# Optimization experiments

Measured on AMD Instinct MI355X. Metric: run time of the kernel, lower is better.

Reference implementation:

```python
import jax, jax.numpy as jnp
import numpy as np

N_HEADS = 8
WINDOW = 4

def setup_inputs() -> dict:
    key = jax.random.key(0)
    ks = jax.random.split(key, 12)
    B, C, L = 8, 512, 1024
    Dh = C // N_HEADS
    s = 1.0 / np.sqrt(C)
    inp = {
        'x': jax.random.normal(ks[0], (B, C, L), dtype=jnp.float32),
        'Wq': jax.random.normal(ks[1], (C, C), dtype=jnp.float32) * s,
        'bq': jnp.zeros((C,), dtype=jnp.float32),
        'Wk': jax.random.normal(ks[2], (C, C), dtype=jnp.float32) * s,
        'bk': jnp.zeros((C,), dtype=jnp.float32),
        'Wv': jax.random.normal(ks[3], (C, C), dtype=jnp.float32) * s,
        'bv': jnp.zeros((C,), dtype=jnp.float32),
        'Wo': jax.random.normal(ks[4], (C, C), dtype=jnp.float32) * s,
        'bo': jnp.zeros((C,), dtype=jnp.float32),
        'emb_rel_k': jax.random.normal(ks[5], (2 * WINDOW + 1, Dh), dtype=jnp.float32) * 0.02,
        'emb_rel_v': jax.random.normal(ks[6], (2 * WINDOW + 1, Dh), dtype=jnp.float32) * 0.02,
    }
    return inp


def reference(x, Wq, bq, Wk, bk, Wv, bv, Wo, bo, emb_rel_k, emb_rel_v):
    B, C, L = x.shape
    H = N_HEADS
    Dh = C // H
    scale = Dh ** -0.5

    def proj(W, b):
        # pointwise conv1d == channel-mixing matmul; (B,C,L) -> (B,H,L,Dh)
        y = jnp.einsum('oc,bcl->bol', W, x) + b[:, None]
        return y.reshape(B, H, Dh, L).transpose(0, 1, 3, 2)

    q = proj(Wq, bq) * scale
    k = proj(Wk, bk)
    v = proj(Wv, bv)

    scores = jnp.einsum('bhld,bhjd->bhlj', q, k)  # (B,H,L,L)

    t = jnp.arange(L)
    diff = t[None, :] - t[:, None]                      # (L,L)
    window_mask = (jnp.abs(diff) <= WINDOW)
    indices = jnp.clip(diff, -WINDOW, WINDOW) + WINDOW  # (L,L) in [0, 2w]

    rel_k = emb_rel_k[indices]                          # (L,L,Dh)
    rel_scores = jnp.einsum('bhld,ljd->bhlj', q, rel_k)
    scores = scores + rel_scores * window_mask[None, None, :, :]

    attn = jax.nn.softmax(scores, axis=-1)

    out = jnp.einsum('bhlj,bhjd->bhld', attn, v)
    rel_v = emb_rel_v[indices] * window_mask[:, :, None]  # (L,L,Dh)
    out = out + jnp.einsum('bhlj,ljd->bhld', attn, rel_v)

    out = out.transpose(0, 1, 3, 2).reshape(B, C, L)
    out = jnp.einsum('oc,bcl->bol', Wo, out) + bo[:, None]
    return out
```

## Files before the change

kernel.cpp:

```cpp
#include <hip/hip_runtime.h>
#include <math.h>

#define B_  8
#define H_  8
#define C_  512
#define L_  1024
#define DH  64
#define WIN 4

typedef __attribute__((ext_vector_type(8))) short short8;
typedef __attribute__((ext_vector_type(4))) float floatx4;

__device__ __forceinline__ unsigned short f2bf(float f) {
    unsigned int u = __float_as_uint(f);
    u = u + 0x7FFFu + ((u >> 16) & 1u);
    return (unsigned short)(u >> 16);
}
__device__ __forceinline__ float bf2f(unsigned short h) {
    return __uint_as_float(((unsigned int)h) << 16);
}
__device__ __forceinline__ unsigned short f2h(float f) {
    _Float16 h = (_Float16)f;
    return *reinterpret_cast<unsigned short*>(&h);
}

__device__ __forceinline__ void gload_lds16(const void* g, void* l) {
    __builtin_amdgcn_global_load_lds(
        (const __attribute__((address_space(1))) void*)g,
        (__attribute__((address_space(3))) void*)l, 16, 0, 0);
}

__global__ __launch_bounds__(256) void prep_kernel(
    const float* __restrict__ Wq, const float* __restrict__ Wk,
    const float* __restrict__ Wv, const float* __restrict__ Wo,
    const float* __restrict__ bq, const float* __restrict__ bk,
    const float* __restrict__ bv,
    unsigned short* __restrict__ Wqkv_hi,
    unsigned short* __restrict__ Wo_h,
    float* __restrict__ bqkv)
{
    const int i = blockIdx.x * 256 + threadIdx.x;
    float4 v; ushort4 h;

    v = ((const float4*)Wq)[i];
    h.x = f2bf(v.x); h.y = f2bf(v.y); h.z = f2bf(v.z); h.w = f2bf(v.w);
    ((ushort4*)Wqkv_hi)[i] = h;

    v = ((const float4*)Wk)[i];
    h.x = f2bf(v.x); h.y = f2bf(v.y); h.z = f2bf(v.z); h.w = f2bf(v.w);
    ((ushort4*)Wqkv_hi)[65536 + i] = h;

    v = ((const float4*)Wv)[i];
    h.x = f2bf(v.x); h.y = f2bf(v.y); h.z = f2bf(v.z); h.w = f2bf(v.w);
    ((ushort4*)Wqkv_hi)[131072 + i] = h;

    v = ((const float4*)Wo)[i];
    h.x = f2h(v.x); h.y = f2h(v.y); h.z = f2h(v.z); h.w = f2h(v.w);
    ((ushort4*)Wo_h)[i] = h;

    if (i < 512)       bqkv[i] = bq[i];
    else if (i < 1024) bqkv[i] = bk[i - 512];
    else if (i < 1536) bqkv[i] = bv[i - 1024];
}

__global__ __launch_bounds__(256) void transpose_kernel(
    const float* __restrict__ x, unsigned short* __restrict__ xT)
{
    __shared__ float tile[32][33];
    const int b  = blockIdx.z;
    const int cb = blockIdx.y * 32;
    const int lb = blockIdx.x * 32;
    const int t  = threadIdx.x;
    {
        const int l = t & 31, c0 = t >> 5;
#pragma unroll
        for (int p = 0; p < 4; ++p) {
            const int c = c0 + 8 * p;
            tile[c][l] = x[((size_t)b * C_ + cb + c) * L_ + lb + l];
        }
    }
    __syncthreads();
    {
        const int c = t & 31, l0 = t >> 5;
#pragma unroll
        for (int p = 0; p < 4; ++p) {
            const int l = l0 + 8 * p;
            xT[((size_t)b * L_ + lb + l) * C_ + cb + c] = f2bf(tile[c][l]);
        }
    }
}

__global__ __launch_bounds__(256) void qkv_gemm_kernel(
    const unsigned short* __restrict__ Wh, const float* __restrict__ bqkv,
    const unsigned short* __restrict__ xT,
    unsigned short* __restrict__ Qb, unsigned short* __restrict__ Kb,
    unsigned short* __restrict__ Vc)
{
    __shared__ __align__(16) unsigned short SM[18432];

    const int b   = blockIdx.z;
    const int oB  = blockIdx.y * 128;
    const int mat = oB >> 9;
    const int ob  = oB & 511;
    const int lb  = blockIdx.x * 128;
    const int t  = threadIdx.x;
    const int w = t >> 6, lane = t & 63, quad = lane >> 4, lc = lane & 15;
    const int wm = w >> 1, wn = w & 1;

    const unsigned short* Wm = Wh + (size_t)mat * C_ * C_;

    floatx4 acc[4][4];
#pragma unroll
    for (int i = 0; i < 4; ++i)
#pragma unroll
        for (int j = 0; j < 4; ++j) acc[i][j] = (floatx4)0.f;

    const int srow = w * 32 + (lane >> 2);
    const int sc8  = (lane & 3) * 8;

#define QKV_STAGE(BUF, S) {                                                  \
    const int c0_ = (S) * 32;                                                \
    _Pragma("unroll")                                                        \
    for (int p_ = 0; p_ < 2; ++p_) {                                         \
        gload_lds16(&Wm[(size_t)(ob + srow + 16 * p_) * C_ + c0_ + sc8],     \
                    &SM[(0 * 2 + (BUF)) * 4096 + (w * 32 + p_ * 16) * 32]);  \
        gload_lds16(&xT[((size_t)b * L_ + lb + srow + 16 * p_) * C_ + c0_ + sc8], \
                    &SM[(1 * 2 + (BUF)) * 4096 + (w * 32 + p_ * 16) * 32]);  \
    }                                                                        \
}

    QKV_STAGE(0, 0)
    __syncthreads();

    for (int s = 0; s < 16; ++s) {
        const int cur = s & 1;
        if (s < 15) QKV_STAGE(1 - cur, s + 1)

        const unsigned short (*At)[32] =
            reinterpret_cast<const unsigned short (*)[32]>(&SM[(0 * 2 + cur) * 4096]);
        const unsigned short (*Bt)[32] =
            reinterpret_cast<const unsigned short (*)[32]>(&SM[(1 * 2 + cur) * 4096]);

        short8 a[4], bb[4];
#pragma unroll
        for (int mt = 0; mt < 4; ++mt)
            a[mt] = *reinterpret_cast<const short8*>(&At[wm * 64 + mt * 16 + lc][quad * 8]);
#pragma unroll
        for (int nt = 0; nt < 4; ++nt)
            bb[nt] = *reinterpret_cast<const short8*>(&Bt[wn * 64 + nt * 16 + lc][quad * 8]);
#pragma unroll
        for (int mt = 0; mt < 4; ++mt)
#pragma unroll
            for (int nt = 0; nt < 4; ++nt)
                acc[mt][nt] = __builtin_amdgcn_mfma_f32_16x16x32_bf16(
                    a[mt], bb[nt], acc[mt][nt], 0, 0, 0);

        __syncthreads();
    }

    if (mat == 2) {
#pragma unroll
        for (int mt = 0; mt < 4; ++mt) {
#pragma unroll
            for (int r = 0; r < 4; ++r) {
                const int o  = ob + wm * 64 + mt * 16 + quad * 4 + r;
                const float bi = bqkv[1024 + o];
#pragma unroll
                for (int nt = 0; nt < 4; ++nt) {
                    const int l = lb + wn * 64 + nt * 16 + lc;
                    Vc[((size_t)b * C_ + o) * L_ + l] = f2bf(acc[mt][nt][r] + bi);
                }
            }
        }
    } else {
        const float scale = (mat == 0) ? 0.125f : 1.0f;
        unsigned short* dst = (mat == 0) ? Qb : Kb;
        unsigned short (*sT)[144] =
            reinterpret_cast<unsigned short (*)[144]>(&SM[0]);

#pragma unroll
        for (int mt = 0; mt < 4; ++mt) {
#pragma unroll
            for (int r = 0; r < 4; ++r) {
                const int o  = ob + wm * 64 + mt * 16 + quad * 4 + r;
                const float bi = bqkv[mat * 512 + o];
                const int d  = mt * 16 + quad * 4 + r;
#pragma unroll
                for (int nt = 0; nt < 4; ++nt) {
                    const int l = wn * 64 + nt * 16 + lc;
                    sT[l][wm * 72 + d] = f2bf((acc[mt][nt][r] + bi) * scale);
                }
            }
        }
        __syncthreads();
        {
            const int l = t >> 1, hf = t & 1;
#pragma unroll
            for (int h01 = 0; h01 < 2; ++h01) {
                const int hgl = (ob >> 6) + h01;
                const size_t o = (((size_t)b * H_ + hgl) * L_ + lb + l) * DH + hf * 32;
                const int cbase = h01 * 72 + hf * 32;
                uint4 v0 = *reinterpret_cast<const uint4*>(&sT[l][cbase]);
                uint4 v1 = *reinterpret_cast<const uint4*>(&sT[l][cbase + 8]);
                uint4 v2 = *reinterpret_cast<const uint4*>(&sT[l][cbase + 16]);
                uint4 v3 = *reinterpret_cast<const uint4*>(&sT[l][cbase + 24]);
                *reinterpret_cast<uint4*>(&dst[o])      = v0;
                *reinterpret_cast<uint4*>(&dst[o + 8])  = v1;
                *reinterpret_cast<uint4*>(&dst[o + 16]) = v2;
                *reinterpret_cast<uint4*>(&dst[o + 24]) = v3;
            }
        }
    }
}

__global__ __launch_bounds__(512, 4) void attn_kernel12(
    const unsigned short* __restrict__ Qb,
    const unsigned short* __restrict__ Kb,
    const unsigned short* __restrict__ Vc,
    const float* __restrict__ erel_k, const float* __restrict__ erel_v,
    unsigned short* __restrict__ AOh)
{
    __shared__ __align__(16) unsigned short kst[2][64][68];
    __shared__ __align__(16) unsigned short vst[2][64][68];
    __shared__ __align__(16) unsigned short Pl[8][16][68];
    __shared__ float rs[128][9];
    __shared__ float rv[128][9];

    const int t  = threadIdx.x;
    const int bh = blockIdx.x;
    const int rt = blockIdx.y;
    const int b = bh >> 3, h = bh & 7;
    const int w = t >> 6, lane = t & 63, quad = lane >> 4, lc = lane & 15;
    const int row0 = rt * 128;
    const int rowW = row0 + w * 16;

    const size_t qkBase = (size_t)bh * L_ * DH;
    const size_t vBase  = ((size_t)b * C_ + h * DH) * L_;

    for (int i = lane; i < 16 * 9; i += 64) rv[w * 16 + i / 9][i % 9] = 0.f;

    short8 af[2];
#pragma unroll
    for (int kk = 0; kk < 2; ++kk)
        af[kk] = *reinterpret_cast<const short8*>(
            &Qb[qkBase + (size_t)(rowW + lc) * DH + kk * 32 + quad * 8]);

    {
        floatx4 rsa = (floatx4)0.f;
        const int drow = (lc < 9) ? lc : 8;
#pragma unroll
        for (int kk = 0; kk < 2; ++kk) {
            short8 bfr;
#pragma unroll
            for (int i = 0; i < 8; ++i)
                bfr[i] = (short)f2bf(erel_k[drow * 64 + kk * 32 + quad * 8 + i]);
            rsa = __builtin_amdgcn_mfma_f32_16x16x32_bf16(af[kk], bfr, rsa, 0, 0, 0);
        }
        if (lc < 9) {
#pragma unroll
            for (int r = 0; r < 4; ++r)
                rs[w * 16 + quad * 4 + r][lc] = rsa[r];
        }
    }

    const int jr = t >> 3, jc = (t & 7) * 8;
    *reinterpret_cast<uint4*>(&kst[0][jr][jc]) =
        *reinterpret_cast<const uint4*>(&Kb[qkBase + (size_t)jr * DH + jc]);
    *reinterpret_cast<uint4*>(&vst[0][jr][jc]) =
        *reinterpret_cast<const uint4*>(&Vc[vBase + (size_t)jr * L_ + jc]);
    __syncthreads();

    short8 ones;
#pragma unroll
    for (int j = 0; j < 8; ++j) ones[j] = (short)0x3F80;

    floatx4 acc_o[4], acc_l = (floatx4)0.f;
#pragma unroll
    for (int nt = 0; nt < 4; ++nt) acc_o[nt] = (floatx4)0.f;

    for (int jt = 0; jt < L_ / 64; ++jt) {
        const int j0  = jt * 64;
        const int cur = jt & 1;

        uint4 pk, pv;
        if (jt < L_ / 64 - 1) {
            const int j0n = j0 + 64;
            pk = *reinterpret_cast<const uint4*>(
                &Kb[qkBase + (size_t)(j0n + jr) * DH + jc]);
            pv = *reinterpret_cast<const uint4*>(
                &Vc[vBase + (size_t)jr * L_ + j0n + jc]);
        }

        floatx4 sacc[4];
#pragma unroll
        for (int nt = 0; nt < 4; ++nt) sacc[nt] = (floatx4)0.f;
#pragma unroll
        for (int nt = 0; nt < 4; ++nt)
#pragma unroll
            for (int kk = 0; kk < 2; ++kk) {
                const short8 kf = *reinterpret_cast<const short8*>(
                    &kst[cur][nt * 16 + lc][kk * 32 + quad * 8]);
                sacc[nt] = __builtin_amdgcn_mfma_f32_16x16x32_bf16(kf, af[kk], sacc[nt], 0, 0, 0);
            }

        const bool nearD = (j0 <= rowW + 15 + WIN) && (j0 + 63 >= rowW - WIN);
        if (nearD) {
#pragma unroll
            for (int nt = 0; nt < 4; ++nt) {
#pragma unroll
                for (int r = 0; r < 4; ++r) {
                    const int diff = (j0 + nt * 16 + quad * 4 + r) - (rowW + lc);
                    if (diff >= -WIN && diff <= WIN)
                        sacc[nt][r] += rs[w * 16 + lc][diff + WIN];
                }
            }
        }

#pragma unroll
        for (int nt = 0; nt < 4; ++nt) {
            const float e0 = __expf(sacc[nt][0]);
            const float e1 = __expf(sacc[nt][1]);
            const float e2 = __expf(sacc[nt][2]);
            const float e3 = __expf(sacc[nt][3]);
            unsigned int u01, u23;
            asm("v_cvt_pk_bf16_f32 %0, %1, %2" : "=v"(u01) : "v"(e0), "v"(e1));
            asm("v_cvt_pk_bf16_f32 %0, %1, %2" : "=v"(u23) : "v"(e2), "v"(e3));
            uint2 pr; pr.x = u01; pr.y = u23;
            *reinterpret_cast<uint2*>(&Pl[w][lc][nt * 16 + quad * 4]) = pr;
        }

        if (nearD) {
            for (int idx = lane; idx < 16 * 9; idx += 64) {
                const int r16 = idx / 9, dr = idx % 9;
                const int jg = rowW + r16 + dr - WIN;
                if (jg >= j0 && jg < j0 + 64 && jg >= 0 && jg < L_)
                    rv[w * 16 + r16][dr] += bf2f(Pl[w][r16][jg - j0]);
            }
        }

        short8 pf[2];
#pragma unroll
        for (int kk = 0; kk < 2; ++kk)
            pf[kk] = *reinterpret_cast<const short8*>(&Pl[w][lc][kk * 32 + quad * 8]);

#pragma unroll
        for (int kk = 0; kk < 2; ++kk)
            acc_l = __builtin_amdgcn_mfma_f32_16x16x32_bf16(pf[kk], ones, acc_l, 0, 0, 0);

#pragma unroll
        for (int nt = 0; nt < 4; ++nt)
#pragma unroll
            for (int kk = 0; kk < 2; ++kk) {
                const short8 vf = *reinterpret_cast<const short8*>(
                    &vst[cur][nt * 16 + lc][kk * 32 + quad * 8]);
                acc_o[nt] = __builtin_amdgcn_mfma_f32_16x16x32_bf16(pf[kk], vf, acc_o[nt], 0, 0, 0);
            }

        if (jt < L_ / 64 - 1) {
            *reinterpret_cast<uint4*>(&kst[1 - cur][jr][jc]) = pk;
            *reinterpret_cast<uint4*>(&vst[1 - cur][jr][jc]) = pv;
        }
        __syncthreads();
    }

#pragma unroll
    for (int nt = 0; nt < 4; ++nt) {
        const int d = nt * 16 + lc;
        float ev[9];
#pragma unroll
        for (int dr = 0; dr < 9; ++dr) ev[dr] = erel_v[dr * 64 + d];
#pragma unroll
        for (int r = 0; r < 4; ++r) {
            const int rloc = w * 16 + quad * 4 + r;
            float v = acc_o[nt][r];
#pragma unroll
            for (int dr = 0; dr < 9; ++dr) v += rv[rloc][dr] * ev[dr];
            Pl[w][quad * 4 + r][nt * 16 + lc] = f2h(v / acc_l[r]);
        }
    }
    {
        const int row = lane >> 2, ds8 = (lane & 3) * 16;
        const uint4 q0 = *reinterpret_cast<const uint4*>(&Pl[w][row][ds8]);
        const uint4 q1 = *reinterpret_cast<const uint4*>(&Pl[w][row][ds8 + 8]);
        const size_t o = ((size_t)b * L_ + rowW + row) * C_ + h * 64 + ds8;
        *reinterpret_cast<uint4*>(&AOh[o])     = q0;
        *reinterpret_cast<uint4*>(&AOh[o + 8]) = q1;
    }
}

__global__ __launch_bounds__(256) void out_gemm_kernel(
    const unsigned short* __restrict__ Wh,
    const float* __restrict__ bo,
    const unsigned short* __restrict__ Ah,
    float* __restrict__ Y)
{
    __shared__ __align__(16) unsigned short Asb[2][128][32];
    __shared__ __align__(16) unsigned short Bsb[2][64][32];

    const int b  = blockIdx.z;
    const int ob = blockIdx.y * 128;
    const int lb = blockIdx.x * 64;
    const int t  = threadIdx.x;
    const int w = t >> 6, lane = t & 63, quad = lane >> 4, lc = lane & 15;
    const int wm = w >> 1, wn = w & 1;

    floatx4 acc[4][2];
#pragma unroll
    for (int i = 0; i < 4; ++i)
#pragma unroll
        for (int j = 0; j < 2; ++j) acc[i][j] = (floatx4)0.f;

    const int srow = (lane >> 2);
    const int sc8  = (lane & 3) * 8;

#define OG_STAGE(BUF, S) {                                                   \
    const int c0_ = (S) * 32;                                                \
    _Pragma("unroll")                                                        \
    for (int p_ = 0; p_ < 2; ++p_)                                           \
        gload_lds16(&Wh[(size_t)(ob + w * 32 + p_ * 16 + srow) * C_ + c0_ + sc8], \
                    &Asb[BUF][w * 32 + p_ * 16][0]);                         \
    gload_lds16(&Ah[((size_t)b * L_ + lb + w * 16 + srow) * C_ + c0_ + sc8], \
                &Bsb[BUF][w * 16][0]);                                       \
}

    OG_STAGE(0, 0)
    __syncthreads();

    for (int s = 0; s < 16; ++s) {
        const int cur = s & 1;
        if (s < 15) OG_STAGE(1 - cur, s + 1)

        short8 ah[4], bhf[2];
#pragma unroll
        for (int mt = 0; mt < 4; ++mt)
            ah[mt] = *reinterpret_cast<const short8*>(
                &Asb[cur][wm * 64 + mt * 16 + lc][quad * 8]);
#pragma unroll
        for (int nt = 0; nt < 2; ++nt)
            bhf[nt] = *reinterpret_cast<const short8*>(
                &Bsb[cur][wn * 32 + nt * 16 + lc][quad * 8]);
#pragma unroll
        for (int mt = 0; mt < 4; ++mt)
#pragma unroll
            for (int nt = 0; nt < 2; ++nt)
                acc[mt][nt] = __builtin_amdgcn_mfma_f32_16x16x32_f16(
                    ah[mt], bhf[nt], acc[mt][nt], 0, 0, 0);

        __syncthreads();
    }

#pragma unroll
    for (int mt = 0; mt < 4; ++mt) {
#pragma unroll
        for (int r = 0; r < 4; ++r) {
            const int o = ob + wm * 64 + mt * 16 + quad * 4 + r;
            const float bi = bo[o];
#pragma unroll
            for (int nt = 0; nt < 2; ++nt) {
                const int l = lb + wn * 32 + nt * 16 + lc;
                Y[((size_t)b * C_ + o) * L_ + l] = acc[mt][nt][r] + bi;
            }
        }
    }
}

extern "C" void kernel_launch(void* const* d_in, const int* in_sizes, int n_in,
                              void* d_out, int out_size, void* d_ws, size_t ws_size,
                              hipStream_t stream)
{
    const float* x   = (const float*)d_in[0];
    const float* Wq  = (const float*)d_in[1];
    const float* bq  = (const float*)d_in[2];
    const float* Wk  = (const float*)d_in[3];
    const float* bk  = (const float*)d_in[4];
    const float* Wv  = (const float*)d_in[5];
    const float* bv  = (const float*)d_in[6];
    const float* Wo  = (const float*)d_in[7];
    const float* bo  = (const float*)d_in[8];
    const float* erk = (const float*)d_in[9];
    const float* erv = (const float*)d_in[10];

    char* ws = (char*)d_ws;
    const size_t MB = 1024u * 1024u;
    unsigned short* xT      = (unsigned short*)(ws);
    unsigned short* Qb      = (unsigned short*)(ws + 8 * MB);
    unsigned short* Kb      = (unsigned short*)(ws + 16 * MB);
    unsigned short* Vc      = (unsigned short*)(ws + 24 * MB);
    unsigned short* AOh     = (unsigned short*)(ws + 32 * MB);
    unsigned short* Wqkv_hi = (unsigned short*)(ws + 40 * MB);
    unsigned short* Wo_h    = (unsigned short*)(ws + 42 * MB);
    float*          bqkv    = (float*)(ws + 43 * MB);

    prep_kernel<<<256, 256, 0, stream>>>(Wq, Wk, Wv, Wo, bq, bk, bv,
                                         Wqkv_hi, Wo_h, bqkv);
    transpose_kernel<<<dim3(L_ / 32, C_ / 32, B_), 256, 0, stream>>>(x, xT);
    qkv_gemm_kernel<<<dim3(L_ / 128, 12, B_), 256, 0, stream>>>(
        Wqkv_hi, bqkv, xT, Qb, Kb, Vc);
    attn_kernel12<<<dim3(64, 8), 512, 0, stream>>>(
        Qb, Kb, Vc, erk, erv, AOh);
    out_gemm_kernel<<<dim3(L_ / 64, C_ / 128, B_), 256, 0, stream>>>(
        Wo_h, bo, AOh, (float*)d_out);
}
```

Before: 167.0 us.

## Process two 16-row query tiles per wave in attention kernel with 256 threads

```diff
diff --git a/kernel.cpp b/kernel.cpp
--- a/kernel.cpp
+++ b/kernel.cpp
@@ -213,7 +213,7 @@
     }
 }
 
-__global__ __launch_bounds__(512, 4) void attn_kernel12(
+__global__ __launch_bounds__(256, 2) void attn_kernel13a(
     const unsigned short* __restrict__ Qb,
     const unsigned short* __restrict__ Kb,
     const unsigned short* __restrict__ Vc,
@@ -222,7 +222,7 @@
 {
     __shared__ __align__(16) unsigned short kst[2][64][68];
     __shared__ __align__(16) unsigned short vst[2][64][68];
-    __shared__ __align__(16) unsigned short Pl[8][16][68];
+    __shared__ __align__(16) unsigned short Pl[4][2][16][68];
     __shared__ float rs[128][9];
     __shared__ float rv[128][9];
 
@@ -231,22 +231,24 @@
     const int rt = blockIdx.y;
     const int b = bh >> 3, h = bh & 7;
     const int w = t >> 6, lane = t & 63, quad = lane >> 4, lc = lane & 15;
-    const int row0 = rt * 128;
-    const int rowW = row0 + w * 16;
+    const int rowB = rt * 128 + w * 32;
 
     const size_t qkBase = (size_t)bh * L_ * DH;
     const size_t vBase  = ((size_t)b * C_ + h * DH) * L_;
 
-    for (int i = lane; i < 16 * 9; i += 64) rv[w * 16 + i / 9][i % 9] = 0.f;
-
-    short8 af[2];
-#pragma unroll
-    for (int kk = 0; kk < 2; ++kk)
-        af[kk] = *reinterpret_cast<const short8*>(
-            &Qb[qkBase + (size_t)(rowW + lc) * DH + kk * 32 + quad * 8]);
+    for (int i = lane; i < 32 * 9; i += 64) rv[w * 32 + i / 9][i % 9] = 0.f;
+
+    short8 af0[2], af1[2];
+#pragma unroll
+    for (int kk = 0; kk < 2; ++kk) {
+        af0[kk] = *reinterpret_cast<const short8*>(
+            &Qb[qkBase + (size_t)(rowB + lc) * DH + kk * 32 + quad * 8]);
+        af1[kk] = *reinterpret_cast<const short8*>(
+            &Qb[qkBase + (size_t)(rowB + 16 + lc) * DH + kk * 32 + quad * 8]);
+    }
 
     {
-        floatx4 rsa = (floatx4)0.f;
+        floatx4 rsa0 = (floatx4)0.f, rsa1 = (floatx4)0.f;
         const int drow = (lc < 9) ? lc : 8;
 #pragma unroll
         for (int kk = 0; kk < 2; ++kk) {
@@ -254,98 +256,150 @@
 #pragma unroll
             for (int i = 0; i < 8; ++i)
                 bfr[i] = (short)f2bf(erel_k[drow * 64 + kk * 32 + quad * 8 + i]);
-            rsa = __builtin_amdgcn_mfma_f32_16x16x32_bf16(af[kk], bfr, rsa, 0, 0, 0);
+            rsa0 = __builtin_amdgcn_mfma_f32_16x16x32_bf16(af0[kk], bfr, rsa0, 0, 0, 0);
+            rsa1 = __builtin_amdgcn_mfma_f32_16x16x32_bf16(af1[kk], bfr, rsa1, 0, 0, 0);
         }
         if (lc < 9) {
 #pragma unroll
-            for (int r = 0; r < 4; ++r)
-                rs[w * 16 + quad * 4 + r][lc] = rsa[r];
-        }
-    }
-
-    const int jr = t >> 3, jc = (t & 7) * 8;
-    *reinterpret_cast<uint4*>(&kst[0][jr][jc]) =
-        *reinterpret_cast<const uint4*>(&Kb[qkBase + (size_t)jr * DH + jc]);
-    *reinterpret_cast<uint4*>(&vst[0][jr][jc]) =
-        *reinterpret_cast<const uint4*>(&Vc[vBase + (size_t)jr * L_ + jc]);
+            for (int r = 0; r < 4; ++r) {
+                rs[w * 32 + quad * 4 + r][lc]      = rsa0[r];
+                rs[w * 32 + 16 + quad * 4 + r][lc] = rsa1[r];
+            }
+        }
+    }
+
+    const int jr = t >> 2, jcE = (t & 3) * 16;
+    *reinterpret_cast<uint4*>(&kst[0][jr][jcE]) =
+        *reinterpret_cast<const uint4*>(&Kb[qkBase + (size_t)jr * DH + jcE]);
+    *reinterpret_cast<uint4*>(&kst[0][jr][jcE + 8]) =
+        *reinterpret_cast<const uint4*>(&Kb[qkBase + (size_t)jr * DH + jcE + 8]);
+    *reinterpret_cast<uint4*>(&vst[0][jr][jcE]) =
+        *reinterpret_cast<const uint4*>(&Vc[vBase + (size_t)jr * L_ + jcE]);
+    *reinterpret_cast<uint4*>(&vst[0][jr][jcE + 8]) =
+        *reinterpret_cast<const uint4*>(&Vc[vBase + (size_t)jr * L_ + jcE + 8]);
     __syncthreads();
 
     short8 ones;
 #pragma unroll
     for (int j = 0; j < 8; ++j) ones[j] = (short)0x3F80;
 
-    floatx4 acc_o[4], acc_l = (floatx4)0.f;
-#pragma unroll
-    for (int nt = 0; nt < 4; ++nt) acc_o[nt] = (floatx4)0.f;
+    floatx4 acc_o0[4], acc_o1[4], acc_l0 = (floatx4)0.f, acc_l1 = (floatx4)0.f;
+#pragma unroll
+    for (int nt = 0; nt < 4; ++nt) { acc_o0[nt] = (floatx4)0.f; acc_o1[nt] = (floatx4)0.f; }
 
     for (int jt = 0; jt < L_ / 64; ++jt) {
         const int j0  = jt * 64;
         const int cur = jt & 1;
 
-        uint4 pk, pv;
+        uint4 pk0, pk1, pv0, pv1;
         if (jt < L_ / 64 - 1) {
             const int j0n = j0 + 64;
-            pk = *reinterpret_cast<const uint4*>(
-                &Kb[qkBase + (size_t)(j0n + jr) * DH + jc]);
-            pv = *reinterpret_cast<const uint4*>(
-                &Vc[vBase + (size_t)jr * L_ + j0n + jc]);
-        }
-
-        floatx4 sacc[4];
-#pragma unroll
-        for (int nt = 0; nt < 4; ++nt) sacc[nt] = (floatx4)0.f;
+            pk0 = *reinterpret_cast<const uint4*>(
+                &Kb[qkBase + (size_t)(j0n + jr) * DH + jcE]);
+            pk1 = *reinterpret_cast<const uint4*>(
+                &Kb[qkBase + (size_t)(j0n + jr) * DH + jcE + 8]);
+            pv0 = *reinterpret_cast<const uint4*>(
+                &Vc[vBase + (size_t)jr * L_ + j0n + jcE]);
+            pv1 = *reinterpret_cast<const uint4*>(
+                &Vc[vBase + (size_t)jr * L_ + j0n + jcE + 8]);
+        }
+
+        floatx4 s0[4], s1[4];
+#pragma unroll
+        for (int nt = 0; nt < 4; ++nt) { s0[nt] = (floatx4)0.f; s1[nt] = (floatx4)0.f; }
 #pragma unroll
         for (int nt = 0; nt < 4; ++nt)
 #pragma unroll
             for (int kk = 0; kk < 2; ++kk) {
                 const short8 kf = *reinterpret_cast<const short8*>(
                     &kst[cur][nt * 16 + lc][kk * 32 + quad * 8]);
-                sacc[nt] = __builtin_amdgcn_mfma_f32_16x16x32_bf16(kf, af[kk], sacc[nt], 0, 0, 0);
-            }
-
-        const bool nearD = (j0 <= rowW + 15 + WIN) && (j0 + 63 >= rowW - WIN);
-        if (nearD) {
+                s0[nt] = __builtin_amdgcn_mfma_f32_16x16x32_bf16(kf, af0[kk], s0[nt], 0, 0, 0);
+                s1[nt] = __builtin_amdgcn_mfma_f32_16x16x32_bf16(kf, af1[kk], s1[nt], 0, 0, 0);
+            }
+
+        short8 pf0[2], pf1[2];
+
+        {
+            const int rowW = rowB;
+            const bool nearD = (j0 <= rowW + 15 + WIN) && (j0 + 63 >= rowW - WIN);
+            if (nearD) {
+#pragma unroll
+                for (int nt = 0; nt < 4; ++nt)
+#pragma unroll
+                    for (int r = 0; r < 4; ++r) {
+                        const int diff = (j0 + nt * 16 + quad * 4 + r) - (rowW + lc);
+                        if (diff >= -WIN && diff <= WIN)
+                            s0[nt][r] += rs[w * 32 + lc][diff + WIN];
+                    }
+            }
 #pragma unroll
             for (int nt = 0; nt < 4; ++nt) {
-#pragma unroll
-                for (int r = 0; r < 4; ++r) {
-                    const int diff = (j0 + nt * 16 + quad * 4 + r) - (rowW + lc);
-                    if (diff >= -WIN && diff <= WIN)
-                        sacc[nt][r] += rs[w * 16 + lc][diff + WIN];
+                const float e0 = __expf(s0[nt][0]);
+                const float e1 = __expf(s0[nt][1]);
+                const float e2 = __expf(s0[nt][2]);
+                const float e3 = __expf(s0[nt][3]);
+                unsigned int u01, u23;
+                asm volatile("v_cvt_pk_bf16_f32 %0, %1, %2" : "=v"(u01) : "v"(e0), "v"(e1));
+                asm volatile("v_cvt_pk_bf16_f32 %0, %1, %2" : "=v"(u23) : "v"(e2), "v"(e3));
+                uint2 pr; pr.x = u01; pr.y = u23;
+                *reinterpret_cast<uint2*>(&Pl[w][0][lc][nt * 16 + quad * 4]) = pr;
+            }
+            if (nearD) {
+                for (int idx = lane; idx < 16 * 9; idx += 64) {
+                    const int r16 = idx / 9, dr = idx % 9;
+                    const int jg = rowW + r16 + dr - WIN;
+                    if (jg >= j0 && jg < j0 + 64 && jg >= 0 && jg < L_)
+                        rv[w * 32 + r16][dr] += bf2f(Pl[w][0][r16][jg - j0]);
                 }
             }
-        }
-
-#pragma unroll
-        for (int nt = 0; nt < 4; ++nt) {
-            const float e0 = __expf(sacc[nt][0]);
-            const float e1 = __expf(sacc[nt][1]);
-            const float e2 = __expf(sacc[nt][2]);
-            const float e3 = __expf(sacc[nt][3]);
-            unsigned int u01, u23;
-            asm("v_cvt_pk_bf16_f32 %0, %1, %2" : "=v"(u01) : "v"(e0), "v"(e1));
-            asm("v_cvt_pk_bf16_f32 %0, %1, %2" : "=v"(u23) : "v"(e2), "v"(e3));
-            uint2 pr; pr.x = u01; pr.y = u23;
-            *reinterpret_cast<uint2*>(&Pl[w][lc][nt * 16 + quad * 4]) = pr;
-        }
-
-        if (nearD) {
-            for (int idx = lane; idx < 16 * 9; idx += 64) {
-                const int r16 = idx / 9, dr = idx % 9;
-                const int jg = rowW + r16 + dr - WIN;
-                if (jg >= j0 && jg < j0 + 64 && jg >= 0 && jg < L_)
-                    rv[w * 16 + r16][dr] += bf2f(Pl[w][r16][jg - j0]);
-            }
-        }
-
-        short8 pf[2];
-#pragma unroll
-        for (int kk = 0; kk < 2; ++kk)
-            pf[kk] = *reinterpret_cast<const short8*>(&Pl[w][lc][kk * 32 + quad * 8]);
-
-#pragma unroll
-        for (int kk = 0; kk < 2; ++kk)
-            acc_l = __builtin_amdgcn_mfma_f32_16x16x32_bf16(pf[kk], ones, acc_l, 0, 0, 0);
+#pragma unroll
+            for (int kk = 0; kk < 2; ++kk)
+                pf0[kk] = *reinterpret_cast<const short8*>(&Pl[w][0][lc][kk * 32 + quad * 8]);
+        }
+
+        {
+            const int rowW = rowB + 16;
+            const bool nearD = (j0 <= rowW + 15 + WIN) && (j0 + 63 >= rowW - WIN);
+            if (nearD) {
+#pragma unroll
+                for (int nt = 0; nt < 4; ++nt)
+#pragma unroll
+                    for (int r = 0; r < 4; ++r) {
+                        const int diff = (j0 + nt * 16 + quad * 4 + r) - (rowW + lc);
+                        if (diff >= -WIN && diff <= WIN)
+                            s1[nt][r] += rs[w * 32 + 16 + lc][diff + WIN];
+                    }
+            }
+#pragma unroll
+            for (int nt = 0; nt < 4; ++nt) {
+                const float e0 = __expf(s1[nt][0]);
+                const float e1 = __expf(s1[nt][1]);
+                const float e2 = __expf(s1[nt][2]);
+                const float e3 = __expf(s1[nt][3]);
+                unsigned int u01, u23;
+                asm volatile("v_cvt_pk_bf16_f32 %0, %1, %2" : "=v"(u01) : "v"(e0), "v"(e1));
+                asm volatile("v_cvt_pk_bf16_f32 %0, %1, %2" : "=v"(u23) : "v"(e2), "v"(e3));
+                uint2 pr; pr.x = u01; pr.y = u23;
+                *reinterpret_cast<uint2*>(&Pl[w][1][lc][nt * 16 + quad * 4]) = pr;
+            }
+            if (nearD) {
+                for (int idx = lane; idx < 16 * 9; idx += 64) {
+                    const int r16 = idx / 9, dr = idx % 9;
+                    const int jg = rowW + r16 + dr - WIN;
+                    if (jg >= j0 && jg < j0 + 64 && jg >= 0 && jg < L_)
+                        rv[w * 32 + 16 + r16][dr] += bf2f(Pl[w][1][r16][jg - j0]);
+                }
+            }
+#pragma unroll
+            for (int kk = 0; kk < 2; ++kk)
+                pf1[kk] = *reinterpret_cast<const short8*>(&Pl[w][1][lc][kk * 32 + quad * 8]);
+        }
+
+#pragma unroll
+        for (int kk = 0; kk < 2; ++kk) {
+            acc_l0 = __builtin_amdgcn_mfma_f32_16x16x32_bf16(pf0[kk], ones, acc_l0, 0, 0, 0);
+            acc_l1 = __builtin_amdgcn_mfma_f32_16x16x32_bf16(pf1[kk], ones, acc_l1, 0, 0, 0);
+        }
 
 #pragma unroll
         for (int nt = 0; nt < 4; ++nt)
@@ -353,36 +407,62 @@
             for (int kk = 0; kk < 2; ++kk) {
                 const short8 vf = *reinterpret_cast<const short8*>(
                     &vst[cur][nt * 16 + lc][kk * 32 + quad * 8]);
-                acc_o[nt] = __builtin_amdgcn_mfma_f32_16x16x32_bf16(pf[kk], vf, acc_o[nt], 0, 0, 0);
+                acc_o0[nt] = __builtin_amdgcn_mfma_f32_16x16x32_bf16(pf0[kk], vf, acc_o0[nt], 0, 0, 0);
+                acc_o1[nt] = __builtin_amdgcn_mfma_f32_16x16x32_bf16(pf1[kk], vf, acc_o1[nt], 0, 0, 0);
             }
 
         if (jt < L_ / 64 - 1) {
-            *reinterpret_cast<uint4*>(&kst[1 - cur][jr][jc]) = pk;
-            *reinterpret_cast<uint4*>(&vst[1 - cur][jr][jc]) = pv;
+            *reinterpret_cast<uint4*>(&kst[1 - cur][jr][jcE])     = pk0;
+            *reinterpret_cast<uint4*>(&kst[1 - cur][jr][jcE + 8]) = pk1;
+            *reinterpret_cast<uint4*>(&vst[1 - cur][jr][jcE])     = pv0;
+            *reinterpret_cast<uint4*>(&vst[1 - cur][jr][jcE + 8]) = pv1;
         }
         __syncthreads();
     }
 
-#pragma unroll
-    for (int nt = 0; nt < 4; ++nt) {
-        const int d = nt * 16 + lc;
-        float ev[9];
-#pragma unroll
-        for (int dr = 0; dr < 9; ++dr) ev[dr] = erel_v[dr * 64 + d];
-#pragma unroll
-        for (int r = 0; r < 4; ++r) {
-            const int rloc = w * 16 + quad * 4 + r;
-            float v = acc_o[nt][r];
-#pragma unroll
-            for (int dr = 0; dr < 9; ++dr) v += rv[rloc][dr] * ev[dr];
-            Pl[w][quad * 4 + r][nt * 16 + lc] = f2h(v / acc_l[r]);
-        }
-    }
     {
+#pragma unroll
+        for (int nt = 0; nt < 4; ++nt) {
+            const int d = nt * 16 + lc;
+            float ev[9];
+#pragma unroll
+            for (int dr = 0; dr < 9; ++dr) ev[dr] = erel_v[dr * 64 + d];
+#pragma unroll
+            for (int r = 0; r < 4; ++r) {
+                const int rloc = w * 32 + quad * 4 + r;
+                float v = acc_o0[nt][r];
+#pragma unroll
+                for (int dr = 0; dr < 9; ++dr) v += rv[rloc][dr] * ev[dr];
+                Pl[w][0][quad * 4 + r][nt * 16 + lc] = f2h(v / acc_l0[r]);
+            }
+        }
         const int row = lane >> 2, ds8 = (lane & 3) * 16;
-        const uint4 q0 = *reinterpret_cast<const uint4*>(&Pl[w][row][ds8]);
-        const uint4 q1 = *reinterpret_cast<const uint4*>(&Pl[w][row][ds8 + 8]);
-        const size_t o = ((size_t)b * L_ + rowW + row) * C_ + h * 64 + ds8;
+        const uint4 q0 = *reinterpret_cast<const uint4*>(&Pl[w][0][row][ds8]);
+        const uint4 q1 = *reinterpret_cast<const uint4*>(&Pl[w][0][row][ds8 + 8]);
+        const size_t o = ((size_t)b * L_ + rowB + row) * C_ + h * 64 + ds8;
+        *reinterpret_cast<uint4*>(&AOh[o])     = q0;
+        *reinterpret_cast<uint4*>(&AOh[o + 8]) = q1;
+    }
+    {
+#pragma unroll
+        for (int nt = 0; nt < 4; ++nt) {
+            const int d = nt * 16 + lc;
+            float ev[9];
+#pragma unroll
+            for (int dr = 0; dr < 9; ++dr) ev[dr] = erel_v[dr * 64 + d];
+#pragma unroll
+            for (int r = 0; r < 4; ++r) {
+                const int rloc = w * 32 + 16 + quad * 4 + r;
+                float v = acc_o1[nt][r];
+#pragma unroll
+                for (int dr = 0; dr < 9; ++dr) v += rv[rloc][dr] * ev[dr];
+                Pl[w][1][quad * 4 + r][nt * 16 + lc] = f2h(v / acc_l1[r]);
+            }
+        }
+        const int row = lane >> 2, ds8 = (lane & 3) * 16;
+        const uint4 q0 = *reinterpret_cast<const uint4*>(&Pl[w][1][row][ds8]);
+        const uint4 q1 = *reinterpret_cast<const uint4*>(&Pl[w][1][row][ds8 + 8]);
+        const size_t o = ((size_t)b * L_ + rowB + 16 + row) * C_ + h * 64 + ds8;
         *reinterpret_cast<uint4*>(&AOh[o])     = q0;
         *reinterpret_cast<uint4*>(&AOh[o + 8]) = q1;
     }
@@ -496,7 +576,7 @@
     transpose_kernel<<<dim3(L_ / 32, C_ / 32, B_), 256, 0, stream>>>(x, xT);
     qkv_gemm_kernel<<<dim3(L_ / 128, 12, B_), 256, 0, stream>>>(
         Wqkv_hi, bqkv, xT, Qb, Kb, Vc);
-    attn_kernel12<<<dim3(64, 8), 512, 0, stream>>>(
+    attn_kernel13a<<<dim3(64, 8), 256, 0, stream>>>(
         Qb, Kb, Vc, erk, erv, AOh);
     out_gemm_kernel<<<dim3(L_ / 64, C_ / 128, B_), 256, 0, stream>>>(
         Wo_h, bo, AOh, (float*)d_out);
```

After: 165.4 us. Within noise of the previous version (-0.9%).
